# Optimization experiments

Hardware: AMD Instinct MI355X
Metric: run time of the kernel (lower is better)

Reference implementation:

```python
import jax, jax.numpy as jnp
import numpy as np

B, T, D, H, S = 512, 256, 128, 128, 32


def _param(key, shape, scale):
    return (jax.random.normal(key, shape, dtype=jnp.float32) * scale)


def setup_inputs() -> dict:
    key = jax.random.key(0)
    ks = jax.random.split(key, 32)
    sD = 1.0 / np.sqrt(D)
    sH = 1.0 / np.sqrt(H)
    inp = {
        'x': jax.random.normal(ks[0], (B, T, D), dtype=jnp.float32),
        'statics': jax.random.normal(ks[1], (B, S), dtype=jnp.float32),
        'mask': (jax.random.uniform(ks[2], (B, T, D)) > 0.5).astype(jnp.float32),
        'delta': jax.random.uniform(ks[3], (B, T, D), dtype=jnp.float32),
        'x_last_observed': jax.random.normal(ks[4], (B, T, D), dtype=jnp.float32),
        'x_mean': jax.random.normal(ks[5], (B, D), dtype=jnp.float32),
        'hs0': jax.random.normal(ks[6], (B, H), dtype=jnp.float32),
        # GRU-D decay params
        'w_dg_x': _param(ks[7], (D,), sD), 'b_dg_x': jnp.zeros((D,), jnp.float32),
        'W_dg_h': _param(ks[8], (H, D), sD), 'b_dg_h': jnp.zeros((H,), jnp.float32),
        # gates: update z, reset r, candidate h
        'W_z': _param(ks[9], (H, D), sD), 'U_z': _param(ks[10], (H, H), sH),
        'V_z': _param(ks[11], (H, D), sD), 'b_z': jnp.zeros((H,), jnp.float32),
        'W_r': _param(ks[12], (H, D), sD), 'U_r': _param(ks[13], (H, H), sH),
        'V_r': _param(ks[14], (H, D), sD), 'b_r': jnp.zeros((H,), jnp.float32),
        'W_h': _param(ks[15], (H, D), sD), 'U_h': _param(ks[16], (H, H), sH),
        'V_h': _param(ks[17], (H, D), sD), 'b_h': jnp.zeros((H,), jnp.float32),
        # classifier
        'W_out': _param(ks[18], (1, H + S), 1.0 / np.sqrt(H + S)),
        'b_out': jnp.zeros((1,), jnp.float32),
    }
    return inp


def reference(x, statics, mask, delta, x_last_observed, x_mean, hs0,
              w_dg_x, b_dg_x, W_dg_h, b_dg_h,
              W_z, U_z, V_z, b_z, W_r, U_r, V_r, b_r,
              W_h, U_h, V_h, b_h, W_out, b_out):
    # scan over time: inputs [T, B, D]
    xs = jnp.transpose(x, (1, 0, 2))
    ms = jnp.transpose(mask, (1, 0, 2))
    ds = jnp.transpose(delta, (1, 0, 2))
    xl = jnp.transpose(x_last_observed, (1, 0, 2))

    def step(h, inputs):
        xv, m, d, xlast = inputs
        gamma_x = jnp.exp(-jax.nn.relu(w_dg_x * d + b_dg_x))            # [B, D]
        gamma_h = jnp.exp(-jax.nn.relu(d @ W_dg_h.T + b_dg_h))          # [B, H]
        x_hat = m * xv + (1.0 - m) * (gamma_x * xlast + (1.0 - gamma_x) * x_mean)
        h = gamma_h * h
        z = jax.nn.sigmoid(x_hat @ W_z.T + h @ U_z.T + m @ V_z.T + b_z)
        r = jax.nn.sigmoid(x_hat @ W_r.T + h @ U_r.T + m @ V_r.T + b_r)
        h_tilde = jnp.tanh(x_hat @ W_h.T + (r * h) @ U_h.T + m @ V_h.T + b_h)
        h = (1.0 - z) * h + z * h_tilde
        return h, None

    h_final, _ = jax.lax.scan(step, hs0, (xs, ms, ds, xl))
    full = jnp.concatenate([h_final, statics], axis=1)                  # [B, H+S]
    predictions = full @ W_out.T + b_out                                # [B, 1]
    return predictions
```

## Files before the change

kernel.cpp:

```cpp
#include <hip/hip_runtime.h>
#include <stdint.h>


#define B_ 512
#define T_ 256
#define D_ 128
#define H_ 128
#define S_ 32
#define NE 512
#define KA 384
#define M_ (B_*T_)
#define HP 136
#define ESLAB ((size_t)NE * 16)
#define ESTRIDE ((size_t)32 * ESLAB)

typedef __attribute__((ext_vector_type(8))) short short8;
typedef __attribute__((ext_vector_type(4))) float f32x4;

__device__ __forceinline__ unsigned short f2bf(float f) {
  union { float f; uint32_t u; } v; v.f = f;
  return (unsigned short)((v.u + 0x7FFFu + ((v.u >> 16) & 1u)) >> 16);
}
__device__ __forceinline__ float bf2f(uint32_t s) {
  union { uint32_t u; float f; } v; v.u = s << 16;
  return v.f;
}

__device__ __forceinline__ uint2  ldraw(const unsigned short* p) { return *(const uint2*)p; }
__device__ __forceinline__ float4 ldraw(const float* p)          { return *(const float4*)p; }
__device__ __forceinline__ void unp(uint2 v, float o[4]) {
  o[0] = bf2f(v.x & 0xffffu); o[1] = bf2f(v.x >> 16);
  o[2] = bf2f(v.y & 0xffffu); o[3] = bf2f(v.y >> 16);
}
__device__ __forceinline__ void unp(float4 v, float o[4]) {
  o[0] = v.x; o[1] = v.y; o[2] = v.z; o[3] = v.w;
}
__device__ __forceinline__ void st4(unsigned short* p, const float v[4]) {
  uint2 u;
  u.x = (uint32_t)f2bf(v[0]) | ((uint32_t)f2bf(v[1]) << 16);
  u.y = (uint32_t)f2bf(v[2]) | ((uint32_t)f2bf(v[3]) << 16);
  *(uint2*)p = u;
}
__device__ __forceinline__ void st4(float* p, const float v[4]) {
  *(float4*)p = make_float4(v[0], v[1], v[2], v[3]);
}

__device__ __forceinline__ float fsigmoid(float x) {
  return __builtin_amdgcn_rcpf(1.f + __expf(-x));
}
__device__ __forceinline__ float ftanh(float x) {
  return 1.f - 2.f * __builtin_amdgcn_rcpf(1.f + __expf(2.f * x));
}

#define ASYNC_CP16(gsrc, ldst) \
  __builtin_amdgcn_global_load_lds((const __attribute__((address_space(1))) void*)(gsrc), \
                                   (__attribute__((address_space(3))) void*)(ldst), 16, 0, 0)

__global__ void prep_weights(const float* __restrict__ Wz, const float* __restrict__ Vz,
                             const float* __restrict__ Wr, const float* __restrict__ Vr,
                             const float* __restrict__ Wh, const float* __restrict__ Vh,
                             const float* __restrict__ Wdgh,
                             const float* __restrict__ bz, const float* __restrict__ br,
                             const float* __restrict__ bh, const float* __restrict__ bdgh,
                             unsigned short* __restrict__ Wcat, float* __restrict__ bias)
{
  int id = blockIdx.x * 256 + threadIdx.x;
  if (id < NE * KA) {
    int n = id / KA, k = id - n * KA;
    float v = 0.f;
    if (n < 384) {
      int nn = n & 127;
      const float* W = (n < 128) ? Wz : (n < 256) ? Wr : Wh;
      const float* V = (n < 128) ? Vz : (n < 256) ? Vr : Vh;
      if (k < 128)      v = W[nn * 128 + k];
      else if (k < 256) v = V[nn * 128 + (k - 128)];
    } else {
      if (k >= 256) v = Wdgh[(n - 384) * 128 + (k - 256)];
    }
    Wcat[id] = f2bf(v);
  }
  if (id < NE) {
    bias[id] = (id < 128) ? bz[id] : (id < 256) ? br[id - 128]
             : (id < 384) ? bh[id - 256] : bdgh[id - 384];
  }
}

__global__ void build_A(const float* __restrict__ x, const float* __restrict__ mask,
                        const float* __restrict__ delta, const float* __restrict__ xlast,
                        const float* __restrict__ xmean,
                        const float* __restrict__ wdgx, const float* __restrict__ bdgx,
                        unsigned short* __restrict__ Abuf)
{
  int id = blockIdx.x * 256 + threadIdx.x;
  int m = id >> 5;
  int c = id & 31;
  int t = m >> 9;
  int b = m & (B_ - 1);
  int k = c * 4;
  size_t src = ((size_t)b * T_ + t) * D_ + k;
  float4 xv = *(const float4*)(x + src);
  float4 mv = *(const float4*)(mask + src);
  float4 dv = *(const float4*)(delta + src);
  float4 lv = *(const float4*)(xlast + src);
  float4 uv = *(const float4*)(xmean + (size_t)b * D_ + k);
  float4 wv = *(const float4*)(wdgx + k);
  float4 bv = *(const float4*)(bdgx + k);
  const float* xp = (const float*)&xv; const float* mp = (const float*)&mv;
  const float* dp = (const float*)&dv; const float* lp = (const float*)&lv;
  const float* up = (const float*)&uv; const float* wp = (const float*)&wv;
  const float* bp = (const float*)&bv;
  unsigned short xh[4], mm[4], dd[4];
  #pragma unroll
  for (int i = 0; i < 4; ++i) {
    float g = __expf(-fmaxf(wp[i] * dp[i] + bp[i], 0.f));
    float xhat = mp[i] * xp[i] + (1.f - mp[i]) * (g * lp[i] + (1.f - g) * up[i]);
    xh[i] = f2bf(xhat); mm[i] = f2bf(mp[i]); dd[i] = f2bf(dp[i]);
  }
  uint2 px, pm, pd;
  px.x = (uint32_t)xh[0] | ((uint32_t)xh[1] << 16); px.y = (uint32_t)xh[2] | ((uint32_t)xh[3] << 16);
  pm.x = (uint32_t)mm[0] | ((uint32_t)mm[1] << 16); pm.y = (uint32_t)mm[2] | ((uint32_t)mm[3] << 16);
  pd.x = (uint32_t)dd[0] | ((uint32_t)dd[1] << 16); pd.y = (uint32_t)dd[2] | ((uint32_t)dd[3] << 16);
  unsigned short* rowp = Abuf + (size_t)m * KA;
  *(uint2*)(rowp + k)       = px;
  *(uint2*)(rowp + 128 + k) = pm;
  *(uint2*)(rowp + 256 + k) = pd;
}

template <typename ET>
__global__ __launch_bounds__(256, 2) void gemm_phase1(
    const unsigned short* __restrict__ Abuf, const unsigned short* __restrict__ Wcat,
    const float* __restrict__ bias, ET* __restrict__ E)
{
  __shared__ unsigned short As[128 * 32];
  __shared__ unsigned short Bs[128 * 32];
  const int tid = threadIdx.x;
  const int wave = tid >> 6, lane = tid & 63;
  const int q = lane >> 4, rl = lane & 15;
  const int m0 = blockIdx.x * 128;
  const int n0 = blockIdx.y * 128;
  const int wm = (wave >> 1) * 64, wn = (wave & 1) * 64;

  f32x4 acc[4][4];
  #pragma unroll
  for (int a = 0; a < 4; ++a)
    #pragma unroll
    for (int b = 0; b < 4; ++b) acc[a][b] = (f32x4){0.f, 0.f, 0.f, 0.f};

  for (int kt = 0; kt < KA / 32; ++kt) {
    const int kbase = kt * 32;
    #pragma unroll
    for (int i = 0; i < 2; ++i) {
      int chunk = i * 256 + wave * 64 + lane;
      int row = chunk >> 2, kc = chunk & 3;
      ASYNC_CP16(Abuf + (size_t)(m0 + row) * KA + kbase + kc * 8,
                 As + (size_t)(i * 256 + wave * 64) * 8);
      ASYNC_CP16(Wcat + (size_t)(n0 + row) * KA + kbase + kc * 8,
                 Bs + (size_t)(i * 256 + wave * 64) * 8);
    }
    __syncthreads();
    short8 af[4], bfr[4];
    #pragma unroll
    for (int tm = 0; tm < 4; ++tm)
      af[tm] = *(const short8*)(As + (wm + tm * 16 + rl) * 32 + q * 8);
    #pragma unroll
    for (int tn = 0; tn < 4; ++tn)
      bfr[tn] = *(const short8*)(Bs + (wn + tn * 16 + rl) * 32 + q * 8);
    #pragma unroll
    for (int tm = 0; tm < 4; ++tm)
      #pragma unroll
      for (int tn = 0; tn < 4; ++tn)
        acc[tm][tn] = __builtin_amdgcn_mfma_f32_16x16x32_bf16(af[tm], bfr[tn], acc[tm][tn], 0, 0, 0);
    __syncthreads();
  }

  const int t = m0 >> 9;
  const int bbase = m0 & (B_ - 1);
  #pragma unroll
  for (int tn = 0; tn < 4; ++tn) {
    int n = n0 + wn + tn * 16 + rl;
    float bv = bias[n];
    bool isg = (n >= 384);
    #pragma unroll
    for (int tm = 0; tm < 4; ++tm) {
      int brow = bbase + wm + tm * 16;
      float v[4];
      #pragma unroll
      for (int reg = 0; reg < 4; ++reg) {
        float xv = acc[tm][tn][reg] + bv;
        v[reg] = isg ? __expf(-fmaxf(xv, 0.f)) : xv;
      }
      st4(E + ((size_t)t * 32 + (brow >> 4)) * ESLAB + (size_t)n * 16 + q * 4, v);
    }
  }
}

template <typename ET>
__global__ __launch_bounds__(512, 2) void grud_scan(
    const ET* __restrict__ E,
    const float* __restrict__ Uz, const float* __restrict__ Ur, const float* __restrict__ Uh,
    const float* __restrict__ hs0, const float* __restrict__ statics,
    const float* __restrict__ Wout, const float* __restrict__ bout,
    float* __restrict__ out)
{
  __shared__ unsigned short hdec[16 * HP];
  __shared__ unsigned short rhb[16 * HP];
  __shared__ float hfin[16 * HP];
  const int tid = threadIdx.x;
  const int wave = tid >> 6, lane = tid & 63;
  const int q = lane >> 4, rl = lane & 15;
  const int col = wave * 16 + rl;
  const int b0 = blockIdx.x * 16;

  short8 uz[4], ur[4], uh[4];
  #pragma unroll
  for (int kc = 0; kc < 4; ++kc) {
    int koff = kc * 32 + q * 8;
    const float* pzw = Uz + col * H_ + koff;
    const float* prw = Ur + col * H_ + koff;
    const float* phw = Uh + col * H_ + koff;
    #pragma unroll
    for (int j = 0; j < 8; ++j) {
      uz[kc][j] = (short)f2bf(pzw[j]);
      ur[kc][j] = (short)f2bf(prw[j]);
      uh[kc][j] = (short)f2bf(phw[j]);
    }
  }

  const ET* pz = E + (size_t)blockIdx.x * ESLAB + (size_t)col * 16 + q * 4;
  const ET* pr = pz + 128 * 16;
  const ET* ph = pz + 256 * 16;
  const ET* pg = pz + 384 * 16;

  using RawT = decltype(ldraw((const ET*)nullptr));
  RawT cz, cr, chh, cg, nz{}, nr{}, nh{}, ng{};
  cz  = ldraw(pz);
  cr  = ldraw(pr);
  chh = ldraw(ph);
  cg  = ldraw(pg + ESTRIDE);
  RawT g0raw = ldraw(pg);

  float hd[4], g0[4];
  unp(g0raw, g0);
  #pragma unroll
  for (int reg = 0; reg < 4; ++reg) {
    int row = q * 4 + reg;
    float h0 = hs0[(b0 + row) * H_ + col];
    hd[reg] = g0[reg] * h0;
    hdec[row * HP + col] = f2bf(hd[reg]);
  }
  __syncthreads();

  for (int t = 0; t < T_; ++t) {
    if (t + 1 < T_) {
      size_t off = (size_t)(t + 1) * ESTRIDE;
      nz = ldraw(pz + off); nr = ldraw(pr + off); nh = ldraw(ph + off);
      if (t + 2 < T_) ng = ldraw(pg + (size_t)(t + 2) * ESTRIDE);
    }
    float Pz[4], Pr[4], Ph[4];
    unp(cz, Pz); unp(cr, Pr); unp(chh, Ph);

    short8 af[4];
    #pragma unroll
    for (int kc = 0; kc < 4; ++kc)
      af[kc] = *(const short8*)(&hdec[rl * HP + kc * 32 + q * 8]);
    f32x4 accz = (f32x4){0.f,0.f,0.f,0.f}, accr = (f32x4){0.f,0.f,0.f,0.f};
    #pragma unroll
    for (int kc = 0; kc < 4; ++kc) {
      accz = __builtin_amdgcn_mfma_f32_16x16x32_bf16(af[kc], uz[kc], accz, 0, 0, 0);
      accr = __builtin_amdgcn_mfma_f32_16x16x32_bf16(af[kc], ur[kc], accr, 0, 0, 0);
    }
    float zz[4];
    #pragma unroll
    for (int reg = 0; reg < 4; ++reg) {
      zz[reg] = fsigmoid(accz[reg] + Pz[reg]);
      float rr = fsigmoid(accr[reg] + Pr[reg]);
      rhb[(q * 4 + reg) * HP + col] = f2bf(rr * hd[reg]);
    }
    __syncthreads();

    short8 ar[4];
    #pragma unroll
    for (int kc = 0; kc < 4; ++kc)
      ar[kc] = *(const short8*)(&rhb[rl * HP + kc * 32 + q * 8]);
    f32x4 acch = (f32x4){0.f,0.f,0.f,0.f};
    #pragma unroll
    for (int kc = 0; kc < 4; ++kc)
      acch = __builtin_amdgcn_mfma_f32_16x16x32_bf16(ar[kc], uh[kc], acch, 0, 0, 0);

    if (t < T_ - 1) {
      float Gn[4];
      unp(cg, Gn);
      #pragma unroll
      for (int reg = 0; reg < 4; ++reg) {
        float ht = ftanh(acch[reg] + Ph[reg]);
        float hn = hd[reg] + zz[reg] * (ht - hd[reg]);
        hd[reg] = Gn[reg] * hn;
        hdec[(q * 4 + reg) * HP + col] = f2bf(hd[reg]);
      }
    } else {
      #pragma unroll
      for (int reg = 0; reg < 4; ++reg) {
        float ht = ftanh(acch[reg] + Ph[reg]);
        float hn = hd[reg] + zz[reg] * (ht - hd[reg]);
        hfin[(q * 4 + reg) * HP + col] = hn;
      }
    }
    __syncthreads();

    cz = nz; cr = nr; chh = nh; cg = ng;
  }

  {
    int row = tid >> 5, j = tid & 31;
    float acc = 0.f;
    #pragma unroll
    for (int c0 = 0; c0 < 4; ++c0)
      acc += hfin[row * HP + j + c0 * 32] * Wout[j + c0 * 32];
    acc += statics[(size_t)(b0 + row) * S_ + j] * Wout[H_ + j];
    #pragma unroll
    for (int off = 16; off >= 1; off >>= 1)
      acc += __shfl_down(acc, off, 32);
    if (j == 0) out[b0 + row] = acc + bout[0];
  }
}

template <typename ET>
static void launch_all(void* const* d_in, float* out, char* ws, hipStream_t stream)
{
  const float* x      = (const float*)d_in[0];
  const float* statics= (const float*)d_in[1];
  const float* mask   = (const float*)d_in[2];
  const float* delta  = (const float*)d_in[3];
  const float* xlast  = (const float*)d_in[4];
  const float* xmean  = (const float*)d_in[5];
  const float* hs0    = (const float*)d_in[6];
  const float* wdgx   = (const float*)d_in[7];
  const float* bdgx   = (const float*)d_in[8];
  const float* Wdgh   = (const float*)d_in[9];
  const float* bdgh   = (const float*)d_in[10];
  const float* Wz     = (const float*)d_in[11];
  const float* Uz     = (const float*)d_in[12];
  const float* Vz     = (const float*)d_in[13];
  const float* bz     = (const float*)d_in[14];
  const float* Wr     = (const float*)d_in[15];
  const float* Ur     = (const float*)d_in[16];
  const float* Vr     = (const float*)d_in[17];
  const float* br     = (const float*)d_in[18];
  const float* Wh     = (const float*)d_in[19];
  const float* Uh     = (const float*)d_in[20];
  const float* Vh     = (const float*)d_in[21];
  const float* bh     = (const float*)d_in[22];
  const float* Wout   = (const float*)d_in[23];
  const float* bout   = (const float*)d_in[24];

  const size_t eBytes = (size_t)M_ * NE * sizeof(ET);
  const size_t aBytes = (size_t)M_ * KA * 2;
  const size_t wBytes = (size_t)NE * KA * 2;
  ET* E = (ET*)ws;
  unsigned short* Abuf = (unsigned short*)(ws + eBytes);
  unsigned short* Wcat = (unsigned short*)(ws + eBytes + aBytes);
  float* bias = (float*)(ws + eBytes + aBytes + wBytes);

  prep_weights<<<768, 256, 0, stream>>>(Wz, Vz, Wr, Vr, Wh, Vh, Wdgh,
                                        bz, br, bh, bdgh, Wcat, bias);
  build_A<<<(M_ * 32) / 256, 256, 0, stream>>>(x, mask, delta, xlast, xmean,
                                               wdgx, bdgx, Abuf);
  gemm_phase1<ET><<<dim3(M_ / 128, NE / 128), 256, 0, stream>>>(Abuf, Wcat, bias, E);
  grud_scan<ET><<<B_ / 16, 512, 0, stream>>>(E, Uz, Ur, Uh, hs0, statics, Wout, bout, out);
}

extern "C" void kernel_launch(void* const* d_in, const int* in_sizes, int n_in,
                              void* d_out, int out_size, void* d_ws, size_t ws_size,
                              hipStream_t stream)
{
  char* ws = (char*)d_ws;
  float* out = (float*)d_out;
  const size_t common = (size_t)M_ * KA * 2 + (size_t)NE * KA * 2 + 4096;
  const size_t needF32 = (size_t)M_ * NE * 4 + common;
  const size_t needBF  = (size_t)M_ * NE * 2 + common;
  if (ws_size >= needF32)     launch_all<float>(d_in, out, ws, stream);
  else if (ws_size >= needBF) launch_all<unsigned short>(d_in, out, ws, stream);
}
```

Baseline: 602.0 us.

## Triple-buffer GEMM k-loop with async copies and lighten scan barriers and bf16 rounding

The phase-1 GEMM now keeps three LDS stages and issues async global-to-LDS copies two k-tiles ahead. It waits with explicit vmcnt counters and one barrier per k-tile instead of two __syncthreads, so load latency can overlap the MFMA work. In the recurrent scan, __syncthreads is replaced by an lgkmcnt wait plus s_barrier that does not drain pending global prefetches, and bf16 conversion switches to cheaper round-half-up. The vmcnt(4) count assumes a fixed number of outstanding copies per stage, and the rounding change slightly alters numerics. The workspace size requirement is also raised.

```diff
diff --git a/kernel.cpp b/kernel.cpp
--- a/kernel.cpp
+++ b/kernel.cpp
@@ -17,9 +17,15 @@
 typedef __attribute__((ext_vector_type(8))) short short8;
 typedef __attribute__((ext_vector_type(4))) float f32x4;
 
+#define BAR_LDS() asm volatile("s_waitcnt lgkmcnt(0)\n\ts_barrier" ::: "memory")
+
 __device__ __forceinline__ unsigned short f2bf(float f) {
   union { float f; uint32_t u; } v; v.f = f;
   return (unsigned short)((v.u + 0x7FFFu + ((v.u >> 16) & 1u)) >> 16);
+}
+__device__ __forceinline__ unsigned short f2bf_fast(float f) {
+  union { float f; uint32_t u; } v; v.f = f;
+  return (unsigned short)((v.u + 0x8000u) >> 16);
 }
 __device__ __forceinline__ float bf2f(uint32_t s) {
   union { uint32_t u; float f; } v; v.u = s << 16;
@@ -131,8 +137,8 @@
     const unsigned short* __restrict__ Abuf, const unsigned short* __restrict__ Wcat,
     const float* __restrict__ bias, ET* __restrict__ E)
 {
-  __shared__ unsigned short As[128 * 32];
-  __shared__ unsigned short Bs[128 * 32];
+  __shared__ unsigned short As[3][4096];
+  __shared__ unsigned short Bs[3][4096];
   const int tid = threadIdx.x;
   const int wave = tid >> 6, lane = tid & 63;
   const int q = lane >> 4, rl = lane & 15;
@@ -146,32 +152,43 @@
     #pragma unroll
     for (int b = 0; b < 4; ++b) acc[a][b] = (f32x4){0.f, 0.f, 0.f, 0.f};
 
-  for (int kt = 0; kt < KA / 32; ++kt) {
-    const int kbase = kt * 32;
-    #pragma unroll
-    for (int i = 0; i < 2; ++i) {
-      int chunk = i * 256 + wave * 64 + lane;
-      int row = chunk >> 2, kc = chunk & 3;
-      ASYNC_CP16(Abuf + (size_t)(m0 + row) * KA + kbase + kc * 8,
-                 As + (size_t)(i * 256 + wave * 64) * 8);
-      ASYNC_CP16(Wcat + (size_t)(n0 + row) * KA + kbase + kc * 8,
-                 Bs + (size_t)(i * 256 + wave * 64) * 8);
-    }
-    __syncthreads();
+  #define STAGE(kt_) do {                                                     \
+    const int kbase_ = (kt_) * 32; const int buf_ = (kt_) % 3;                \
+    _Pragma("unroll")                                                         \
+    for (int i = 0; i < 2; ++i) {                                             \
+      int chunk = i * 256 + wave * 64 + lane;                                 \
+      int row = chunk >> 2, kc = chunk & 3;                                   \
+      ASYNC_CP16(Abuf + (size_t)(m0 + row) * KA + kbase_ + kc * 8,            \
+                 &As[buf_][(i * 256 + wave * 64) * 8]);                       \
+      ASYNC_CP16(Wcat + (size_t)(n0 + row) * KA + kbase_ + kc * 8,            \
+                 &Bs[buf_][(i * 256 + wave * 64) * 8]);                       \
+    }                                                                         \
+  } while (0)
+
+  STAGE(0);
+  STAGE(1);
+
+  #pragma unroll
+  for (int kt = 0; kt < 12; ++kt) {
+    if (kt == 11) asm volatile("s_waitcnt vmcnt(0)" ::: "memory");
+    else          asm volatile("s_waitcnt vmcnt(4)" ::: "memory");
+    asm volatile("s_barrier" ::: "memory");
+    if (kt < 10) STAGE(kt + 2);
+    const int buf = kt % 3;
     short8 af[4], bfr[4];
     #pragma unroll
     for (int tm = 0; tm < 4; ++tm)
-      af[tm] = *(const short8*)(As + (wm + tm * 16 + rl) * 32 + q * 8);
+      af[tm] = *(const short8*)(&As[buf][(wm + tm * 16 + rl) * 32 + q * 8]);
     #pragma unroll
     for (int tn = 0; tn < 4; ++tn)
-      bfr[tn] = *(const short8*)(Bs + (wn + tn * 16 + rl) * 32 + q * 8);
+      bfr[tn] = *(const short8*)(&Bs[buf][(wn + tn * 16 + rl) * 32 + q * 8]);
     #pragma unroll
     for (int tm = 0; tm < 4; ++tm)
       #pragma unroll
       for (int tn = 0; tn < 4; ++tn)
         acc[tm][tn] = __builtin_amdgcn_mfma_f32_16x16x32_bf16(af[tm], bfr[tn], acc[tm][tn], 0, 0, 0);
-    __syncthreads();
-  }
+  }
+  #undef STAGE
 
   const int t = m0 >> 9;
   const int bbase = m0 & (B_ - 1);
@@ -246,9 +263,9 @@
     int row = q * 4 + reg;
     float h0 = hs0[(b0 + row) * H_ + col];
     hd[reg] = g0[reg] * h0;
-    hdec[row * HP + col] = f2bf(hd[reg]);
-  }
-  __syncthreads();
+    hdec[row * HP + col] = f2bf_fast(hd[reg]);
+  }
+  BAR_LDS();
 
   for (int t = 0; t < T_; ++t) {
     if (t + 1 < T_) {
@@ -274,9 +291,9 @@
     for (int reg = 0; reg < 4; ++reg) {
       zz[reg] = fsigmoid(accz[reg] + Pz[reg]);
       float rr = fsigmoid(accr[reg] + Pr[reg]);
-      rhb[(q * 4 + reg) * HP + col] = f2bf(rr * hd[reg]);
-    }
-    __syncthreads();
+      rhb[(q * 4 + reg) * HP + col] = f2bf_fast(rr * hd[reg]);
+    }
+    BAR_LDS();
 
     short8 ar[4];
     #pragma unroll
@@ -295,7 +312,7 @@
         float ht = ftanh(acch[reg] + Ph[reg]);
         float hn = hd[reg] + zz[reg] * (ht - hd[reg]);
         hd[reg] = Gn[reg] * hn;
-        hdec[(q * 4 + reg) * HP + col] = f2bf(hd[reg]);
+        hdec[(q * 4 + reg) * HP + col] = f2bf_fast(hd[reg]);
       }
     } else {
       #pragma unroll
@@ -305,7 +322,7 @@
         hfin[(q * 4 + reg) * HP + col] = hn;
       }
     }
-    __syncthreads();
+    BAR_LDS();
 
     cz = nz; cr = nr; chh = nh; cg = ng;
   }
@@ -375,7 +392,7 @@
 {
   char* ws = (char*)d_ws;
   float* out = (float*)d_out;
-  const size_t common = (size_t)M_ * KA * 2 + (size_t)NE * KA * 2 + 4096;
+  const size_t common = (size_t)M_ * KA * 2 + (size_t)NE * KA * 2 + 8192;
   const size_t needF32 = (size_t)M_ * NE * 4 + common;
   const size_t needBF  = (size_t)M_ * NE * 2 + common;
   if (ws_size >= needF32)     launch_all<float>(d_in, out, ws, stream);
```

After: 597.5 us. No clear change (-0.8%).
